# Performance work log

Measured on AMD Instinct MI355X. Metric: run time of the kernel, lower is better.

The kernel has to match this reference:

```python
import jax, jax.numpy as jnp
import numpy as np

N = 8192
NUM_CLASSES = 81            # background + 80 fg classes (COCO)
SCORE_THRESH = 0.05
NMS_THRESH = 0.5
NUM_DETECTIONS = 100
REG_W = (10.0, 10.0, 5.0, 5.0)
MIN_SIZE = 1.0
BBOX_XFORM_CLIP = float(np.log(1000.0 / 16.0))


def setup_inputs() -> dict:
    key = jax.random.key(0)
    k1, k2, k3, k4 = jax.random.split(key, 4)
    xy1 = jax.random.uniform(k1, (N, 2), minval=0.0, maxval=700.0)
    wh = jax.random.uniform(k2, (N, 2), minval=8.0, maxval=300.0)
    proposal = jnp.concatenate([xy1, xy1 + wh], axis=1)          # [N,4] xyxy
    class_logit = jax.random.normal(k3, (N, NUM_CLASSES), dtype=jnp.float32)
    box_regression = jax.random.normal(k4, (N, NUM_CLASSES * 4), dtype=jnp.float32) * 0.5
    return {"proposal": proposal, "class_logit": class_logit,
            "box_regression": box_regression, "image_h": 800, "image_w": 1216}


def _decode(deltas, boxes):
    # deltas [..., N, 4] (per-class), boxes [N, 4] xyxy; standard Fast R-CNN BoxCoder.decode
    wx, wy, ww, wh = REG_W
    widths = boxes[:, 2] - boxes[:, 0]
    heights = boxes[:, 3] - boxes[:, 1]
    cx = boxes[:, 0] + 0.5 * widths
    cy = boxes[:, 1] + 0.5 * heights
    dx = deltas[..., 0] / wx
    dy = deltas[..., 1] / wy
    dw = jnp.minimum(deltas[..., 2] / ww, BBOX_XFORM_CLIP)
    dh = jnp.minimum(deltas[..., 3] / wh, BBOX_XFORM_CLIP)
    pcx = dx * widths + cx
    pcy = dy * heights + cy
    pw = jnp.exp(dw) * widths
    ph = jnp.exp(dh) * heights
    return jnp.stack([pcx - 0.5 * pw, pcy - 0.5 * ph,
                      pcx + 0.5 * pw, pcy + 0.5 * ph], axis=-1)


def _iou_one(box, boxes):
    # IoU of one box [4] against all boxes [N,4]
    lt = jnp.maximum(box[:2], boxes[:, :2])
    rb = jnp.minimum(box[2:], boxes[:, 2:])
    whc = jnp.clip(rb - lt, 0.0)
    inter = whc[:, 0] * whc[:, 1]
    a1 = (box[2] - box[0]) * (box[3] - box[1])
    a2 = (boxes[:, 2] - boxes[:, 0]) * (boxes[:, 3] - boxes[:, 1])
    return inter / (a1 + a2 - inter + 1e-12)


def _nms_per_class(boxes, scores):
    # Sequential greedy NMS: pick highest score, suppress IoU>thresh, repeat.
    # boxes [N,4], scores [N] (already 0 where filtered). Returns top NUM_DETECTIONS.
    def step(scores_w, _):
        j = jnp.argmax(scores_w)
        s = scores_w[j]
        valid = s > 0.0
        bj = boxes[j]
        iou = _iou_one(bj, boxes)                         # [N]
        new = jnp.where(iou > NMS_THRESH, 0.0, scores_w).at[j].set(0.0)
        new = jnp.where(valid, new, scores_w)
        return new, (bj, s, valid)
    _, (sel_b, sel_s, sel_v) = jax.lax.scan(step, scores, None, length=NUM_DETECTIONS)
    return sel_b, sel_s, sel_v                            # [D,4], [D], [D]


def reference(proposal, class_logit, box_regression, image_h, image_w):
    pred_score = jax.nn.softmax(class_logit, axis=-1)     # [N, C]
    deltas = box_regression.reshape(N, NUM_CLASSES, 4)
    fg_deltas = jnp.transpose(deltas[:, 1:, :], (1, 0, 2))  # [C-1, N, 4]
    boxes = _decode(fg_deltas, proposal)                    # [C-1, N, 4]
    # clip to image (process_box)
    W = jnp.float32(image_w); H = jnp.float32(image_h)
    x1 = jnp.clip(boxes[..., 0], 0.0, W)
    y1 = jnp.clip(boxes[..., 1], 0.0, H)
    x2 = jnp.clip(boxes[..., 2], 0.0, W)
    y2 = jnp.clip(boxes[..., 3], 0.0, H)
    boxes = jnp.stack([x1, y1, x2, y2], axis=-1)            # [C-1, N, 4]
    keep_size = ((x2 - x1) >= MIN_SIZE) & ((y2 - y1) >= MIN_SIZE)
    scores = jnp.transpose(pred_score[:, 1:])               # [C-1, N]
    scores = jnp.where((scores >= SCORE_THRESH) & keep_size, scores, 0.0)
    sel_b, sel_s, sel_v = jax.vmap(_nms_per_class)(boxes, scores)  # [C-1,D,...]
    out_boxes = sel_b.reshape(-1, 4)                         # [(C-1)*D, 4]
    out_scores = sel_s.reshape(-1)
    out_labels = jnp.repeat(jnp.arange(1, NUM_CLASSES, dtype=jnp.int32), NUM_DETECTIONS)
    out_valid = sel_v.reshape(-1)
    return out_boxes, out_scores, out_labels, out_valid
```

## Files before the change

kernel.cpp:

```cpp
#include <hip/hip_runtime.h>
#include <hip/hip_bf16.h>

#define NN 8192
#define NC 81
#define FG 80
#define ND 100
#define SH 8
#define CAPS 128
#define CPADI 32
#define MAXK 384
#define KW6 6
#define KROW 8
#define BBOX_CLIP 4.135166556742356f

__global__ __launch_bounds__(256) void decode_kernel(
    const float* __restrict__ prop,
    const float* __restrict__ logit,
    const float* __restrict__ reg,
    const int* __restrict__ ih, const int* __restrict__ iw,
    int* __restrict__ counts,
    float* __restrict__ boxes0,
    float* __restrict__ cbox,
    float* __restrict__ cscore)
{
    const int n = blockIdx.x * 4 + (threadIdx.x >> 6);
    const int shard = blockIdx.x & (SH - 1);
    const int lane = threadIdx.x & 63;
    const float* lrow = logit + (long)n * NC;

    float v1 = lrow[lane];
    float v2 = (lane < NC - 64) ? lrow[64 + lane] : -1e30f;
    float m = fmaxf(v1, v2);
#pragma unroll
    for (int off = 32; off; off >>= 1) m = fmaxf(m, __shfl_xor(m, off));
    float e = expf(v1 - m) + ((lane < NC - 64) ? expf(v2 - m) : 0.0f);
#pragma unroll
    for (int off = 32; off; off >>= 1) e += __shfl_xor(e, off);

    const float W = (float)iw[0];
    const float H = (float)ih[0];
    const float4 p = *(const float4*)(prop + n * 4);
    const float pw = p.z - p.x, ph = p.w - p.y;
    const float pcx = p.x + 0.5f * pw, pcy = p.y + 0.5f * ph;

    for (int c = 1 + lane; c <= FG; c += 64) {
        float score = expf(lrow[c] - m) / e;
        const float4 d = *(const float4*)(reg + (long)n * (NC * 4) + c * 4);
        float dx = d.x / 10.0f;
        float dy = d.y / 10.0f;
        float dw = fminf(d.z / 5.0f, BBOX_CLIP);
        float dh = fminf(d.w / 5.0f, BBOX_CLIP);
        float ncx = dx * pw + pcx;
        float ncy = dy * ph + pcy;
        float nw = expf(dw) * pw;
        float nh = expf(dh) * ph;
        float bx1 = ncx - 0.5f * nw, by1 = ncy - 0.5f * nh;
        float bx2 = ncx + 0.5f * nw, by2 = ncy + 0.5f * nh;
        bx1 = fminf(fmaxf(bx1, 0.0f), W);
        by1 = fminf(fmaxf(by1, 0.0f), H);
        bx2 = fminf(fmaxf(bx2, 0.0f), W);
        by2 = fminf(fmaxf(by2, 0.0f), H);
        bool keep = ((bx2 - bx1) >= 1.0f) && ((by2 - by1) >= 1.0f);

        if (n == 0) {
            float* b0 = boxes0 + (c - 1) * 4;
            b0[0] = bx1; b0[1] = by1; b0[2] = bx2; b0[3] = by2;
        }
        if (score >= 0.05f && keep) {
            const int slot = (c - 1) * SH + shard;
            int pos = atomicAdd(&counts[slot * CPADI], 1);
            if (pos < CAPS) {
                float* cb = cbox + ((long)slot * CAPS + pos) * 4;
                cb[0] = bx1; cb[1] = by1; cb[2] = bx2; cb[3] = by2;
                cscore[slot * CAPS + pos] = score;
            }
        }
    }
}

__global__ __launch_bounds__(1024) void nms_kernel(
    const int* __restrict__ counts,
    const float* __restrict__ boxes0,
    const float* __restrict__ cbox,
    const float* __restrict__ cscore,
    float* __restrict__ out)
{
    __shared__ __align__(16) float  s_sc[MAXK];
    __shared__ float4 s_ubox[MAXK];
    __shared__ int    s_sidx[MAXK];
    __shared__ float4 s_box[MAXK];
    __shared__ float  s_ss[MAXK];
    __shared__ unsigned long long s_row[MAXK * KROW];

    const int c = blockIdx.x;
    const int t = threadIdx.x;
    const int lane = t & 63;
    const int wv = t >> 6;

    int cnt0 = min(counts[(c * SH + 0) * CPADI], CAPS);
    int cnt1 = min(counts[(c * SH + 1) * CPADI], CAPS);
    int cnt2 = min(counts[(c * SH + 2) * CPADI], CAPS);
    int cnt3 = min(counts[(c * SH + 3) * CPADI], CAPS);
    int cnt4 = min(counts[(c * SH + 4) * CPADI], CAPS);
    int cnt5 = min(counts[(c * SH + 5) * CPADI], CAPS);
    int cnt6 = min(counts[(c * SH + 6) * CPADI], CAPS);
    int cnt7 = min(counts[(c * SH + 7) * CPADI], CAPS);
    int K = cnt0 + cnt1 + cnt2 + cnt3 + cnt4 + cnt5 + cnt6 + cnt7;
    if (K > MAXK) K = MAXK;
    const int KW = (K + 63) >> 6;

    for (int i = t; i < MAXK * KROW; i += 1024) s_row[i] = 0ull;
    for (int i = K + t; i < MAXK; i += 1024) {
        s_sc[i] = 0.0f;
        s_ss[i] = 0.0f;
        s_box[i] = make_float4(0.f, 0.f, 0.f, 0.f);
    }
    {
        const int s = t >> 7;
        const int i = t & (CAPS - 1);
        int mycnt = cnt0;
        if (s == 1) mycnt = cnt1; if (s == 2) mycnt = cnt2;
        if (s == 3) mycnt = cnt3; if (s == 4) mycnt = cnt4;
        if (s == 5) mycnt = cnt5; if (s == 6) mycnt = cnt6;
        if (s == 7) mycnt = cnt7;
        int offs = 0;
        if (s > 0) offs += cnt0; if (s > 1) offs += cnt1;
        if (s > 2) offs += cnt2; if (s > 3) offs += cnt3;
        if (s > 4) offs += cnt4; if (s > 5) offs += cnt5;
        if (s > 6) offs += cnt6;
        if (i < mycnt) {
            int d = offs + i;
            if (d < MAXK) {
                const long src = (long)(c * SH + s) * CAPS + i;
                s_sc[d] = cscore[src];
                s_ubox[d] = *(const float4*)(cbox + src * 4);
            }
        }
    }
    __syncthreads();

    if (t < K) {
        const float si = s_sc[t];
        const float4* s4 = (const float4*)s_sc;
        const int nch = (K + 3) >> 2;
        int r = 0;
        for (int ch = 0; ch < nch; ++ch) {
            const float4 sj = s4[ch];
            const int j = ch * 4;
            r += (sj.x > si) || (sj.x == si && (j + 0) < t);
            r += (sj.y > si) || (sj.y == si && (j + 1) < t);
            r += (sj.z > si) || (sj.z == si && (j + 2) < t);
            r += (sj.w > si) || (sj.w == si && (j + 3) < t);
        }
        s_sidx[r] = t;
    }
    __syncthreads();

    if (t < K) {
        const int i = s_sidx[t];
        s_box[t] = s_ubox[i];
        s_ss[t] = s_sc[i];
    }
    __syncthreads();

    float4 colb[KW6];
    float a2c[KW6];
#pragma unroll
    for (int w = 0; w < KW6; ++w) {
        const float4 b = s_box[w * 64 + lane];
        colb[w] = b;
        a2c[w] = (b.z - b.x) * (b.w - b.y);
    }

    for (int r = wv; r < K; r += 16) {
        const float4 rb = s_box[r];
        const float a1 = (rb.z - rb.x) * (rb.w - rb.y);
        const int w0 = r >> 6;
#pragma unroll
        for (int w = 0; w < KW6; ++w) {
            if (w >= w0 && w < KW) {
                const int j = w * 64 + lane;
                const float lx = fmaxf(rb.x, colb[w].x);
                const float ly = fmaxf(rb.y, colb[w].y);
                const float rx = fminf(rb.z, colb[w].z);
                const float ry = fminf(rb.w, colb[w].w);
                const float cw = fmaxf(rx - lx, 0.0f);
                const float ch = fmaxf(ry - ly, 0.0f);
                const float inter = cw * ch;
                const float iou = inter / (a1 + a2c[w] - inter + 1e-12f);
                const bool sup = (iou > 0.5f) && (j > r);
                const unsigned long long msk = __ballot(sup);
                if (lane == 0) s_row[r * KROW + w] = msk;
            }
        }
    }
    __syncthreads();

    if (wv != 0) return;

    float* ob = out + (long)c * ND * 4;
    float* os = out + (long)FG * ND * 4 + c * ND;
    float* ol = os + FG * ND;
    float* ov = ol + FG * ND;
    const float lab = (float)(c + 1);

    unsigned long long aw0, aw1, aw2, aw3, aw4, aw5;
#define INIW(W) ((K >= (W)*64 + 64) ? ~0ull : ((K <= (W)*64) ? 0ull : ((~0ull) >> (64 - (K - (W)*64)))))
    aw0 = INIW(0); aw1 = INIW(1); aw2 = INIW(2);
    aw3 = INIW(3); aw4 = INIW(4); aw5 = INIW(5);
#undef INIW

    int kept = 0;
#define SWEEP(W, AW)                                                        \
    while (AW != 0 && kept < ND) {                                          \
        const int b_ = __builtin_ctzll(AW);                                 \
        const int i_ = (W) * 64 + b_;                                       \
        const unsigned long long* rp_ = s_row + i_ * KROW;                  \
        unsigned long long q0_ = rp_[0], q1_ = rp_[1], q2_ = rp_[2],        \
                           q3_ = rp_[3], q4_ = rp_[4], q5_ = rp_[5];        \
        if (lane == 0) {                                                    \
            const float4 kb = s_box[i_];                                    \
            ob[kept * 4 + 0] = kb.x; ob[kept * 4 + 1] = kb.y;               \
            ob[kept * 4 + 2] = kb.z; ob[kept * 4 + 3] = kb.w;               \
            os[kept] = s_ss[i_]; ol[kept] = lab; ov[kept] = 1.0f;           \
        }                                                                   \
        kept++;                                                             \
        aw0 &= ~q0_; aw1 &= ~q1_; aw2 &= ~q2_;                              \
        aw3 &= ~q3_; aw4 &= ~q4_; aw5 &= ~q5_;                              \
        AW &= ~(1ull << b_);   \
    }
    SWEEP(0, aw0) SWEEP(1, aw1) SWEEP(2, aw2)
    SWEEP(3, aw3) SWEEP(4, aw4) SWEEP(5, aw5)
#undef SWEEP

    const float b0x1 = boxes0[c * 4 + 0], b0y1 = boxes0[c * 4 + 1];
    const float b0x2 = boxes0[c * 4 + 2], b0y2 = boxes0[c * 4 + 3];
    for (int d = kept + lane; d < ND; d += 64) {
        ob[d * 4 + 0] = b0x1; ob[d * 4 + 1] = b0y1;
        ob[d * 4 + 2] = b0x2; ob[d * 4 + 3] = b0y2;
        os[d] = 0.0f; ol[d] = lab; ov[d] = 0.0f;
    }
}

extern "C" void kernel_launch(void* const* d_in, const int* in_sizes, int n_in,
                              void* d_out, int out_size, void* d_ws, size_t ws_size,
                              hipStream_t stream) {
    const float* prop  = (const float*)d_in[0];
    const float* logit = (const float*)d_in[1];
    const float* reg   = (const float*)d_in[2];
    const int*   ih    = (const int*)d_in[3];
    const int*   iw    = (const int*)d_in[4];
    float* out = (float*)d_out;

    char* ws = (char*)d_ws;
    int*   counts = (int*)ws;
    float* boxes0 = (float*)(ws + 81920);
    float* cscore = (float*)(ws + 90112);
    float* cbox   = (float*)(ws + 90112 + (size_t)FG * SH * CAPS * 4);

    hipMemsetAsync(counts, 0, FG * SH * CPADI * sizeof(int), stream);
    decode_kernel<<<NN / 4, 256, 0, stream>>>(prop, logit, reg, ih, iw,
                                              counts, boxes0, cbox, cscore);
    nms_kernel<<<FG, 1024, 0, stream>>>(counts, boxes0, cbox, cscore, out);
}
```

Before: 116.2 us.

## Replace atomic candidate compaction with dense score matrix and in-NMS box re-decode

The first kernel now writes a dense, transposed [class, N] score matrix (zero where filtered) through a shared-memory transpose, instead of atomically appending boxes and scores into sharded per-class buckets. The NMS kernel scans all N scores of its class with ballot/popcount to compact candidates in index order, then re-decodes only the surviving boxes from the proposals and regression. This removes the memset, the atomics and the candidate box writes. In exchange each NMS block reads 32 KB of scores and does scattered gathers, and the NMS block size drops from 1024 to 512 threads.

```diff
diff --git a/kernel.cpp b/kernel.cpp
--- a/kernel.cpp
+++ b/kernel.cpp
@@ -5,27 +5,42 @@
 #define NC 81
 #define FG 80
 #define ND 100
-#define SH 8
-#define CAPS 128
-#define CPADI 32
 #define MAXK 384
-#define KW6 6
 #define KROW 8
 #define BBOX_CLIP 4.135166556742356f
 
-__global__ __launch_bounds__(256) void decode_kernel(
+__device__ __forceinline__ float4 decode_clip_box(
+    const float4 p, const float4 d, const float W, const float H)
+{
+    const float pw = p.z - p.x, ph = p.w - p.y;
+    const float pcx = p.x + 0.5f * pw, pcy = p.y + 0.5f * ph;
+    const float dx = d.x / 10.0f;
+    const float dy = d.y / 10.0f;
+    const float dw = fminf(d.z / 5.0f, BBOX_CLIP);
+    const float dh = fminf(d.w / 5.0f, BBOX_CLIP);
+    const float ncx = dx * pw + pcx;
+    const float ncy = dy * ph + pcy;
+    const float nw = expf(dw) * pw;
+    const float nh = expf(dh) * ph;
+    float4 b;
+    b.x = fminf(fmaxf(ncx - 0.5f * nw, 0.0f), W);
+    b.y = fminf(fmaxf(ncy - 0.5f * nh, 0.0f), H);
+    b.z = fminf(fmaxf(ncx + 0.5f * nw, 0.0f), W);
+    b.w = fminf(fmaxf(ncy + 0.5f * nh, 0.0f), H);
+    return b;
+}
+
+__global__ __launch_bounds__(1024) void score_kernel(
     const float* __restrict__ prop,
     const float* __restrict__ logit,
     const float* __restrict__ reg,
     const int* __restrict__ ih, const int* __restrict__ iw,
-    int* __restrict__ counts,
-    float* __restrict__ boxes0,
-    float* __restrict__ cbox,
-    float* __restrict__ cscore)
+    float* __restrict__ dscore)
 {
-    const int n = blockIdx.x * 4 + (threadIdx.x >> 6);
-    const int shard = blockIdx.x & (SH - 1);
+    __shared__ float s_tr[16 * FG];
+    const int wv = threadIdx.x >> 6;
     const int lane = threadIdx.x & 63;
+    const int n = blockIdx.x * 16 + wv;
     const float* lrow = logit + (long)n * NC;
 
     float v1 = lrow[lane];
@@ -40,102 +55,83 @@
     const float W = (float)iw[0];
     const float H = (float)ih[0];
     const float4 p = *(const float4*)(prop + n * 4);
-    const float pw = p.z - p.x, ph = p.w - p.y;
-    const float pcx = p.x + 0.5f * pw, pcy = p.y + 0.5f * ph;
 
     for (int c = 1 + lane; c <= FG; c += 64) {
-        float score = expf(lrow[c] - m) / e;
+        const float score = expf(lrow[c] - m) / e;
         const float4 d = *(const float4*)(reg + (long)n * (NC * 4) + c * 4);
-        float dx = d.x / 10.0f;
-        float dy = d.y / 10.0f;
-        float dw = fminf(d.z / 5.0f, BBOX_CLIP);
-        float dh = fminf(d.w / 5.0f, BBOX_CLIP);
-        float ncx = dx * pw + pcx;
-        float ncy = dy * ph + pcy;
-        float nw = expf(dw) * pw;
-        float nh = expf(dh) * ph;
-        float bx1 = ncx - 0.5f * nw, by1 = ncy - 0.5f * nh;
-        float bx2 = ncx + 0.5f * nw, by2 = ncy + 0.5f * nh;
-        bx1 = fminf(fmaxf(bx1, 0.0f), W);
-        by1 = fminf(fmaxf(by1, 0.0f), H);
-        bx2 = fminf(fmaxf(bx2, 0.0f), W);
-        by2 = fminf(fmaxf(by2, 0.0f), H);
-        bool keep = ((bx2 - bx1) >= 1.0f) && ((by2 - by1) >= 1.0f);
-
-        if (n == 0) {
-            float* b0 = boxes0 + (c - 1) * 4;
-            b0[0] = bx1; b0[1] = by1; b0[2] = bx2; b0[3] = by2;
-        }
-        if (score >= 0.05f && keep) {
-            const int slot = (c - 1) * SH + shard;
-            int pos = atomicAdd(&counts[slot * CPADI], 1);
-            if (pos < CAPS) {
-                float* cb = cbox + ((long)slot * CAPS + pos) * 4;
-                cb[0] = bx1; cb[1] = by1; cb[2] = bx2; cb[3] = by2;
-                cscore[slot * CAPS + pos] = score;
-            }
-        }
-    }
-}
-
-__global__ __launch_bounds__(1024) void nms_kernel(
-    const int* __restrict__ counts,
-    const float* __restrict__ boxes0,
-    const float* __restrict__ cbox,
-    const float* __restrict__ cscore,
+        const float4 b = decode_clip_box(p, d, W, H);
+        const bool keep = ((b.z - b.x) >= 1.0f) && ((b.w - b.y) >= 1.0f);
+        s_tr[wv * FG + (c - 1)] = (score >= 0.05f && keep) ? score : 0.0f;
+    }
+    __syncthreads();
+
+    const int t = threadIdx.x;
+    if (t < FG * 4) {
+        const int q = t >> 2, pp = t & 3;
+        float4 v;
+        v.x = s_tr[(pp * 4 + 0) * FG + q];
+        v.y = s_tr[(pp * 4 + 1) * FG + q];
+        v.z = s_tr[(pp * 4 + 2) * FG + q];
+        v.w = s_tr[(pp * 4 + 3) * FG + q];
+        *(float4*)(dscore + (long)q * NN + blockIdx.x * 16 + pp * 4) = v;
+    }
+}
+
+__global__ __launch_bounds__(512) void nms_kernel(
+    const float* __restrict__ prop,
+    const float* __restrict__ reg,
+    const int* __restrict__ ih, const int* __restrict__ iw,
+    const float* __restrict__ dscore,
     float* __restrict__ out)
 {
-    __shared__ __align__(16) float  s_sc[MAXK];
-    __shared__ float4 s_ubox[MAXK];
+    __shared__ __align__(16) float s_sc[MAXK];
+    __shared__ int    s_idx[MAXK];
     __shared__ int    s_sidx[MAXK];
+    __shared__ float  s_ss[MAXK];
     __shared__ float4 s_box[MAXK];
-    __shared__ float  s_ss[MAXK];
     __shared__ unsigned long long s_row[MAXK * KROW];
+    __shared__ int s_wb[9];
 
     const int c = blockIdx.x;
     const int t = threadIdx.x;
     const int lane = t & 63;
     const int wv = t >> 6;
-
-    int cnt0 = min(counts[(c * SH + 0) * CPADI], CAPS);
-    int cnt1 = min(counts[(c * SH + 1) * CPADI], CAPS);
-    int cnt2 = min(counts[(c * SH + 2) * CPADI], CAPS);
-    int cnt3 = min(counts[(c * SH + 3) * CPADI], CAPS);
-    int cnt4 = min(counts[(c * SH + 4) * CPADI], CAPS);
-    int cnt5 = min(counts[(c * SH + 5) * CPADI], CAPS);
-    int cnt6 = min(counts[(c * SH + 6) * CPADI], CAPS);
-    int cnt7 = min(counts[(c * SH + 7) * CPADI], CAPS);
-    int K = cnt0 + cnt1 + cnt2 + cnt3 + cnt4 + cnt5 + cnt6 + cnt7;
+    const float W = (float)iw[0];
+    const float H = (float)ih[0];
+    const float* sc_c = dscore + (long)c * NN;
+
+    int wcnt = 0;
+    for (int k = 0; k < 16; ++k) {
+        const int i = wv * 1024 + k * 64 + lane;
+        wcnt += __popcll(__ballot(sc_c[i] > 0.0f));
+    }
+    if (lane == 0) s_wb[wv] = wcnt;
+    __syncthreads();
+    if (t == 0) {
+        int acc = 0;
+        for (int w = 0; w < 8; ++w) { const int x = s_wb[w]; s_wb[w] = acc; acc += x; }
+        s_wb[8] = acc;
+    }
+    __syncthreads();
+    int K = s_wb[8];
     if (K > MAXK) K = MAXK;
     const int KW = (K + 63) >> 6;
 
-    for (int i = t; i < MAXK * KROW; i += 1024) s_row[i] = 0ull;
-    for (int i = K + t; i < MAXK; i += 1024) {
-        s_sc[i] = 0.0f;
-        s_ss[i] = 0.0f;
+    for (int i = t; i < MAXK * KROW; i += 512) s_row[i] = 0ull;
+    for (int i = K + t; i < MAXK; i += 512) {
+        s_sc[i] = 0.0f; s_ss[i] = 0.0f;
         s_box[i] = make_float4(0.f, 0.f, 0.f, 0.f);
     }
-    {
-        const int s = t >> 7;
-        const int i = t & (CAPS - 1);
-        int mycnt = cnt0;
-        if (s == 1) mycnt = cnt1; if (s == 2) mycnt = cnt2;
-        if (s == 3) mycnt = cnt3; if (s == 4) mycnt = cnt4;
-        if (s == 5) mycnt = cnt5; if (s == 6) mycnt = cnt6;
-        if (s == 7) mycnt = cnt7;
-        int offs = 0;
-        if (s > 0) offs += cnt0; if (s > 1) offs += cnt1;
-        if (s > 2) offs += cnt2; if (s > 3) offs += cnt3;
-        if (s > 4) offs += cnt4; if (s > 5) offs += cnt5;
-        if (s > 6) offs += cnt6;
-        if (i < mycnt) {
-            int d = offs + i;
-            if (d < MAXK) {
-                const long src = (long)(c * SH + s) * CAPS + i;
-                s_sc[d] = cscore[src];
-                s_ubox[d] = *(const float4*)(cbox + src * 4);
-            }
-        }
+
+    int base = s_wb[wv];
+    for (int k = 0; k < 16; ++k) {
+        const int i = wv * 1024 + k * 64 + lane;
+        const float s = sc_c[i];
+        const bool pr = s > 0.0f;
+        const unsigned long long mk = __ballot(pr);
+        const int pos = base + __popcll(mk & ((1ull << lane) - 1ull));
+        if (pr && pos < MAXK) { s_sc[pos] = s; s_idx[pos] = i; }
+        base += __popcll(mk);
     }
     __syncthreads();
 
@@ -158,41 +154,39 @@
 
     if (t < K) {
         const int i = s_sidx[t];
-        s_box[t] = s_ubox[i];
         s_ss[t] = s_sc[i];
-    }
-    __syncthreads();
-
-    float4 colb[KW6];
-    float a2c[KW6];
-#pragma unroll
-    for (int w = 0; w < KW6; ++w) {
-        const float4 b = s_box[w * 64 + lane];
-        colb[w] = b;
-        a2c[w] = (b.z - b.x) * (b.w - b.y);
-    }
-
-    for (int r = wv; r < K; r += 16) {
+        const int n = s_idx[i];
+        const float4 p = *(const float4*)(prop + n * 4);
+        const float4 d = *(const float4*)(reg + (long)n * (NC * 4) + (c + 1) * 4);
+        s_box[t] = decode_clip_box(p, d, W, H);
+    }
+    __syncthreads();
+
+    float4 CB0, CB1, CB2, CB3, CB4, CB5;
+    float A0, A1, A2, A3, A4, A5;
+#define LC(Wd, CB, AA) { CB = s_box[(Wd) * 64 + lane]; AA = (CB.z - CB.x) * (CB.w - CB.y); }
+    LC(0, CB0, A0) LC(1, CB1, A1) LC(2, CB2, A2)
+    LC(3, CB3, A3) LC(4, CB4, A4) LC(5, CB5, A5)
+#undef LC
+
+    for (int r = wv; r < K; r += 8) {
         const float4 rb = s_box[r];
-        const float a1 = (rb.z - rb.x) * (rb.w - rb.y);
+        const float ar = (rb.z - rb.x) * (rb.w - rb.y);
         const int w0 = r >> 6;
-#pragma unroll
-        for (int w = 0; w < KW6; ++w) {
-            if (w >= w0 && w < KW) {
-                const int j = w * 64 + lane;
-                const float lx = fmaxf(rb.x, colb[w].x);
-                const float ly = fmaxf(rb.y, colb[w].y);
-                const float rx = fminf(rb.z, colb[w].z);
-                const float ry = fminf(rb.w, colb[w].w);
-                const float cw = fmaxf(rx - lx, 0.0f);
-                const float ch = fmaxf(ry - ly, 0.0f);
-                const float inter = cw * ch;
-                const float iou = inter / (a1 + a2c[w] - inter + 1e-12f);
-                const bool sup = (iou > 0.5f) && (j > r);
-                const unsigned long long msk = __ballot(sup);
-                if (lane == 0) s_row[r * KROW + w] = msk;
-            }
+#define DW(Wd, CB, AA)                                                       \
+        if ((Wd) >= w0 && (Wd) < KW) {                                       \
+            const float lx = fmaxf(rb.x, CB.x), ly = fmaxf(rb.y, CB.y);      \
+            const float rx = fminf(rb.z, CB.z), ry = fminf(rb.w, CB.w);      \
+            const float cw = fmaxf(rx - lx, 0.0f), ch = fmaxf(ry - ly, 0.0f);\
+            const float inter = cw * ch;                                     \
+            const float iou = inter / (ar + AA - inter + 1e-12f);            \
+            const bool sup = (iou > 0.5f) && ((Wd) * 64 + lane > r);         \
+            const unsigned long long mk = __ballot(sup);                     \
+            if (lane == 0) s_row[r * KROW + (Wd)] = mk;                      \
         }
+        DW(0, CB0, A0) DW(1, CB1, A1) DW(2, CB2, A2)
+        DW(3, CB3, A3) DW(4, CB4, A4) DW(5, CB5, A5)
+#undef DW
     }
     __syncthreads();
 
@@ -205,16 +199,16 @@
     const float lab = (float)(c + 1);
 
     unsigned long long aw0, aw1, aw2, aw3, aw4, aw5;
-#define INIW(W) ((K >= (W)*64 + 64) ? ~0ull : ((K <= (W)*64) ? 0ull : ((~0ull) >> (64 - (K - (W)*64)))))
+#define INIW(Wd) ((K >= (Wd)*64 + 64) ? ~0ull : ((K <= (Wd)*64) ? 0ull : ((~0ull) >> (64 - (K - (Wd)*64)))))
     aw0 = INIW(0); aw1 = INIW(1); aw2 = INIW(2);
     aw3 = INIW(3); aw4 = INIW(4); aw5 = INIW(5);
 #undef INIW
 
     int kept = 0;
-#define SWEEP(W, AW)                                                        \
+#define SWEEP(Wd, AW)                                                       \
     while (AW != 0 && kept < ND) {                                          \
         const int b_ = __builtin_ctzll(AW);                                 \
-        const int i_ = (W) * 64 + b_;                                       \
+        const int i_ = (Wd) * 64 + b_;                                      \
         const unsigned long long* rp_ = s_row + i_ * KROW;                  \
         unsigned long long q0_ = rp_[0], q1_ = rp_[1], q2_ = rp_[2],        \
                            q3_ = rp_[3], q4_ = rp_[4], q5_ = rp_[5];        \
@@ -227,18 +221,21 @@
         kept++;                                                             \
         aw0 &= ~q0_; aw1 &= ~q1_; aw2 &= ~q2_;                              \
         aw3 &= ~q3_; aw4 &= ~q4_; aw5 &= ~q5_;                              \
-        AW &= ~(1ull << b_);   \
+        AW &= ~(1ull << b_);    \
     }
     SWEEP(0, aw0) SWEEP(1, aw1) SWEEP(2, aw2)
     SWEEP(3, aw3) SWEEP(4, aw4) SWEEP(5, aw5)
 #undef SWEEP
 
-    const float b0x1 = boxes0[c * 4 + 0], b0y1 = boxes0[c * 4 + 1];
-    const float b0x2 = boxes0[c * 4 + 2], b0y2 = boxes0[c * 4 + 3];
-    for (int d = kept + lane; d < ND; d += 64) {
-        ob[d * 4 + 0] = b0x1; ob[d * 4 + 1] = b0y1;
-        ob[d * 4 + 2] = b0x2; ob[d * 4 + 3] = b0y2;
-        os[d] = 0.0f; ol[d] = lab; ov[d] = 0.0f;
+    {
+        const float4 p0 = *(const float4*)(prop);
+        const float4 d0 = *(const float4*)(reg + (c + 1) * 4);
+        const float4 b0 = decode_clip_box(p0, d0, W, H);
+        for (int dd = kept + lane; dd < ND; dd += 64) {
+            ob[dd * 4 + 0] = b0.x; ob[dd * 4 + 1] = b0.y;
+            ob[dd * 4 + 2] = b0.z; ob[dd * 4 + 3] = b0.w;
+            os[dd] = 0.0f; ol[dd] = lab; ov[dd] = 0.0f;
+        }
     }
 }
 
@@ -252,14 +249,8 @@
     const int*   iw    = (const int*)d_in[4];
     float* out = (float*)d_out;
 
-    char* ws = (char*)d_ws;
-    int*   counts = (int*)ws;
-    float* boxes0 = (float*)(ws + 81920);
-    float* cscore = (float*)(ws + 90112);
-    float* cbox   = (float*)(ws + 90112 + (size_t)FG * SH * CAPS * 4);
-
-    hipMemsetAsync(counts, 0, FG * SH * CPADI * sizeof(int), stream);
-    decode_kernel<<<NN / 4, 256, 0, stream>>>(prop, logit, reg, ih, iw,
-                                              counts, boxes0, cbox, cscore);
-    nms_kernel<<<FG, 1024, 0, stream>>>(counts, boxes0, cbox, cscore, out);
-}
+    float* dscore = (float*)d_ws;
+
+    score_kernel<<<NN / 16, 1024, 0, stream>>>(prop, logit, reg, ih, iw, dscore);
+    nms_kernel<<<FG, 512, 0, stream>>>(prop, reg, ih, iw, dscore, out);
+}
```

Result: slower. 123.6 us (+6.4%).

## Replace NMS suppression bitmask matrix with greedy kept-box check in one wave

Applied to the files above, without the earlier changes.

The NMS kernel no longer builds a full KxK IoU suppression bitmask in shared memory. Instead a single wave walks the score-sorted candidates and tests each one against the boxes kept so far, which are held in lane registers (up to 128). The block shrinks from 1024 to 256 threads, and the setup loops are strided to match. This removes the O(K^2) IoU work and the 24KB shared bitmask, but turns the greedy pass into a serial loop with a ballot on every candidate.

```diff
diff --git a/kernel.cpp b/kernel.cpp
--- a/kernel.cpp
+++ b/kernel.cpp
@@ -9,8 +9,6 @@
 #define CAPS 128
 #define CPADI 32
 #define MAXK 384
-#define KW6 6
-#define KROW 8
 #define BBOX_CLIP 4.135166556742356f
 
 __global__ __launch_bounds__(256) void decode_kernel(
@@ -78,58 +76,44 @@
     }
 }
 
-__global__ __launch_bounds__(1024) void nms_kernel(
+__global__ __launch_bounds__(256) void nms_kernel(
     const int* __restrict__ counts,
     const float* __restrict__ boxes0,
     const float* __restrict__ cbox,
     const float* __restrict__ cscore,
     float* __restrict__ out)
 {
-    __shared__ __align__(16) float  s_sc[MAXK];
+    __shared__ __align__(16) float s_sc[MAXK];
     __shared__ float4 s_ubox[MAXK];
     __shared__ int    s_sidx[MAXK];
     __shared__ float4 s_box[MAXK];
     __shared__ float  s_ss[MAXK];
-    __shared__ unsigned long long s_row[MAXK * KROW];
+    __shared__ int    s_off[SH + 1];
 
     const int c = blockIdx.x;
     const int t = threadIdx.x;
     const int lane = t & 63;
     const int wv = t >> 6;
 
-    int cnt0 = min(counts[(c * SH + 0) * CPADI], CAPS);
-    int cnt1 = min(counts[(c * SH + 1) * CPADI], CAPS);
-    int cnt2 = min(counts[(c * SH + 2) * CPADI], CAPS);
-    int cnt3 = min(counts[(c * SH + 3) * CPADI], CAPS);
-    int cnt4 = min(counts[(c * SH + 4) * CPADI], CAPS);
-    int cnt5 = min(counts[(c * SH + 5) * CPADI], CAPS);
-    int cnt6 = min(counts[(c * SH + 6) * CPADI], CAPS);
-    int cnt7 = min(counts[(c * SH + 7) * CPADI], CAPS);
-    int K = cnt0 + cnt1 + cnt2 + cnt3 + cnt4 + cnt5 + cnt6 + cnt7;
-    if (K > MAXK) K = MAXK;
-    const int KW = (K + 63) >> 6;
-
-    for (int i = t; i < MAXK * KROW; i += 1024) s_row[i] = 0ull;
-    for (int i = K + t; i < MAXK; i += 1024) {
-        s_sc[i] = 0.0f;
-        s_ss[i] = 0.0f;
-        s_box[i] = make_float4(0.f, 0.f, 0.f, 0.f);
-    }
-    {
-        const int s = t >> 7;
-        const int i = t & (CAPS - 1);
-        int mycnt = cnt0;
-        if (s == 1) mycnt = cnt1; if (s == 2) mycnt = cnt2;
-        if (s == 3) mycnt = cnt3; if (s == 4) mycnt = cnt4;
-        if (s == 5) mycnt = cnt5; if (s == 6) mycnt = cnt6;
-        if (s == 7) mycnt = cnt7;
-        int offs = 0;
-        if (s > 0) offs += cnt0; if (s > 1) offs += cnt1;
-        if (s > 2) offs += cnt2; if (s > 3) offs += cnt3;
-        if (s > 4) offs += cnt4; if (s > 5) offs += cnt5;
-        if (s > 6) offs += cnt6;
-        if (i < mycnt) {
-            int d = offs + i;
+    if (t == 0) {
+        int acc = 0;
+        for (int s = 0; s < SH; ++s) {
+            s_off[s] = acc;
+            acc += min(counts[(c * SH + s) * CPADI], CAPS);
+        }
+        s_off[SH] = acc;
+    }
+    __syncthreads();
+    const int K = min(s_off[SH], MAXK);
+
+    for (int i = K + t; i < MAXK; i += 256) s_sc[i] = 0.0f;
+
+    for (int sl = t; sl < SH * CAPS; sl += 256) {
+        const int s = sl >> 7;
+        const int i = sl & (CAPS - 1);
+        const int cnt = s_off[s + 1] - s_off[s];
+        if (i < cnt) {
+            const int d = s_off[s] + i;
             if (d < MAXK) {
                 const long src = (long)(c * SH + s) * CAPS + i;
                 s_sc[d] = cscore[src];
@@ -139,60 +123,27 @@
     }
     __syncthreads();
 
-    if (t < K) {
-        const float si = s_sc[t];
+    for (int i = t; i < K; i += 256) {
+        const float si = s_sc[i];
         const float4* s4 = (const float4*)s_sc;
         const int nch = (K + 3) >> 2;
         int r = 0;
         for (int ch = 0; ch < nch; ++ch) {
             const float4 sj = s4[ch];
             const int j = ch * 4;
-            r += (sj.x > si) || (sj.x == si && (j + 0) < t);
-            r += (sj.y > si) || (sj.y == si && (j + 1) < t);
-            r += (sj.z > si) || (sj.z == si && (j + 2) < t);
-            r += (sj.w > si) || (sj.w == si && (j + 3) < t);
-        }
-        s_sidx[r] = t;
-    }
-    __syncthreads();
-
-    if (t < K) {
-        const int i = s_sidx[t];
-        s_box[t] = s_ubox[i];
-        s_ss[t] = s_sc[i];
-    }
-    __syncthreads();
-
-    float4 colb[KW6];
-    float a2c[KW6];
-#pragma unroll
-    for (int w = 0; w < KW6; ++w) {
-        const float4 b = s_box[w * 64 + lane];
-        colb[w] = b;
-        a2c[w] = (b.z - b.x) * (b.w - b.y);
-    }
-
-    for (int r = wv; r < K; r += 16) {
-        const float4 rb = s_box[r];
-        const float a1 = (rb.z - rb.x) * (rb.w - rb.y);
-        const int w0 = r >> 6;
-#pragma unroll
-        for (int w = 0; w < KW6; ++w) {
-            if (w >= w0 && w < KW) {
-                const int j = w * 64 + lane;
-                const float lx = fmaxf(rb.x, colb[w].x);
-                const float ly = fmaxf(rb.y, colb[w].y);
-                const float rx = fminf(rb.z, colb[w].z);
-                const float ry = fminf(rb.w, colb[w].w);
-                const float cw = fmaxf(rx - lx, 0.0f);
-                const float ch = fmaxf(ry - ly, 0.0f);
-                const float inter = cw * ch;
-                const float iou = inter / (a1 + a2c[w] - inter + 1e-12f);
-                const bool sup = (iou > 0.5f) && (j > r);
-                const unsigned long long msk = __ballot(sup);
-                if (lane == 0) s_row[r * KROW + w] = msk;
-            }
-        }
+            r += (sj.x > si) || (sj.x == si && (j + 0) < i);
+            r += (sj.y > si) || (sj.y == si && (j + 1) < i);
+            r += (sj.z > si) || (sj.z == si && (j + 2) < i);
+            r += (sj.w > si) || (sj.w == si && (j + 3) < i);
+        }
+        s_sidx[r] = i;
+    }
+    __syncthreads();
+
+    for (int r = t; r < K; r += 256) {
+        const int i = s_sidx[r];
+        s_box[r] = s_ubox[i];
+        s_ss[r] = s_sc[i];
     }
     __syncthreads();
 
@@ -204,34 +155,49 @@
     float* ov = ol + FG * ND;
     const float lab = (float)(c + 1);
 
-    unsigned long long aw0, aw1, aw2, aw3, aw4, aw5;
-#define INIW(W) ((K >= (W)*64 + 64) ? ~0ull : ((K <= (W)*64) ? 0ull : ((~0ull) >> (64 - (K - (W)*64)))))
-    aw0 = INIW(0); aw1 = INIW(1); aw2 = INIW(2);
-    aw3 = INIW(3); aw4 = INIW(4); aw5 = INIW(5);
-#undef INIW
+    float4 KB0 = make_float4(0.f, 0.f, 0.f, 0.f);
+    float4 KB1 = make_float4(0.f, 0.f, 0.f, 0.f);
+    float KA0 = 0.0f, KA1 = 0.0f;
 
     int kept = 0;
-#define SWEEP(W, AW)                                                        \
-    while (AW != 0 && kept < ND) {                                          \
-        const int b_ = __builtin_ctzll(AW);                                 \
-        const int i_ = (W) * 64 + b_;                                       \
-        const unsigned long long* rp_ = s_row + i_ * KROW;                  \
-        unsigned long long q0_ = rp_[0], q1_ = rp_[1], q2_ = rp_[2],        \
-                           q3_ = rp_[3], q4_ = rp_[4], q5_ = rp_[5];        \
-        if (lane == 0) {                                                    \
-            const float4 kb = s_box[i_];                                    \
-            ob[kept * 4 + 0] = kb.x; ob[kept * 4 + 1] = kb.y;               \
-            ob[kept * 4 + 2] = kb.z; ob[kept * 4 + 3] = kb.w;               \
-            os[kept] = s_ss[i_]; ol[kept] = lab; ov[kept] = 1.0f;           \
-        }                                                                   \
-        kept++;                                                             \
-        aw0 &= ~q0_; aw1 &= ~q1_; aw2 &= ~q2_;                              \
-        aw3 &= ~q3_; aw4 &= ~q4_; aw5 &= ~q5_;                              \
-        AW &= ~(1ull << b_);   \
-    }
-    SWEEP(0, aw0) SWEEP(1, aw1) SWEEP(2, aw2)
-    SWEEP(3, aw3) SWEEP(4, aw4) SWEEP(5, aw5)
-#undef SWEEP
+    float4 nb = (K > 0) ? s_box[0] : make_float4(0.f, 0.f, 0.f, 0.f);
+    for (int i = 0; i < K; ++i) {
+        if (kept >= ND) break;
+        const float4 cb = nb;
+        nb = s_box[(i + 1 < K) ? i + 1 : i];
+        const float ca = (cb.z - cb.x) * (cb.w - cb.y);
+
+        bool sup;
+        {
+            const float lx = fmaxf(cb.x, KB0.x), ly = fmaxf(cb.y, KB0.y);
+            const float rx = fminf(cb.z, KB0.z), ry = fminf(cb.w, KB0.w);
+            const float w = fmaxf(rx - lx, 0.0f), h = fmaxf(ry - ly, 0.0f);
+            const float inter = w * h;
+            const float iou = inter / (ca + KA0 - inter + 1e-12f);
+            sup = (lane < kept) && (iou > 0.5f);
+        }
+        if (kept > 64) {
+            const float lx = fmaxf(cb.x, KB1.x), ly = fmaxf(cb.y, KB1.y);
+            const float rx = fminf(cb.z, KB1.z), ry = fminf(cb.w, KB1.w);
+            const float w = fmaxf(rx - lx, 0.0f), h = fmaxf(ry - ly, 0.0f);
+            const float inter = w * h;
+            const float iou = inter / (ca + KA1 - inter + 1e-12f);
+            sup = sup || ((lane + 64 < kept) && (iou > 0.5f));
+        }
+        if (__ballot(sup) == 0ull) {
+            if (kept < 64) {
+                if (lane == kept) { KB0 = cb; KA0 = ca; }
+            } else {
+                if (lane == kept - 64) { KB1 = cb; KA1 = ca; }
+            }
+            if (lane == 0) {
+                ob[kept * 4 + 0] = cb.x; ob[kept * 4 + 1] = cb.y;
+                ob[kept * 4 + 2] = cb.z; ob[kept * 4 + 3] = cb.w;
+                os[kept] = s_ss[i]; ol[kept] = lab; ov[kept] = 1.0f;
+            }
+            ++kept;
+        }
+    }
 
     const float b0x1 = boxes0[c * 4 + 0], b0y1 = boxes0[c * 4 + 1];
     const float b0x2 = boxes0[c * 4 + 2], b0y2 = boxes0[c * 4 + 3];
@@ -261,5 +227,5 @@
     hipMemsetAsync(counts, 0, FG * SH * CPADI * sizeof(int), stream);
     decode_kernel<<<NN / 4, 256, 0, stream>>>(prop, logit, reg, ih, iw,
                                               counts, boxes0, cbox, cscore);
-    nms_kernel<<<FG, 1024, 0, stream>>>(counts, boxes0, cbox, cscore, out);
+    nms_kernel<<<FG, 256, 0, stream>>>(counts, boxes0, cbox, cscore, out);
 }
```

After: 128.1 us. +10.2%, slower.
